# Kernel tuning notes

Measured on AMD Instinct MI355X. Metric: run time of the kernel, lower is better.

The kernel has to match this reference:

```python
import jax, jax.numpy as jnp
import numpy as np

N = 100000   # nodes_num
E = 1600000  # nnz edges (avg degree 16)
F = 256      # input_dim
D = 128      # output_dim
LEAKY_SLOPE = 0.2  # tf.nn.leaky_relu default alpha


def setup_inputs() -> dict:
    key = jax.random.key(0)
    ks = jax.random.split(key, 10)
    x = jax.random.normal(ks[0], (N, F), dtype=jnp.float32)
    adj_vals = jnp.ones((E,), dtype=jnp.float32)
    W_map = jax.random.normal(ks[1], (F, D), dtype=jnp.float32) * 0.05
    w1 = jax.random.normal(ks[2], (D,), dtype=jnp.float32) * 0.05
    b1 = jnp.zeros((1,), dtype=jnp.float32)
    w2 = jax.random.normal(ks[3], (D,), dtype=jnp.float32) * 0.05
    b2 = jnp.zeros((1,), dtype=jnp.float32)
    kernel = jax.random.normal(ks[4], (F, D), dtype=jnp.float32) * 0.05
    bias = jax.random.normal(ks[5], (N, D), dtype=jnp.float32) * 0.05
    edge_row = jnp.sort(jax.random.randint(ks[6], (E,), 0, N, dtype=jnp.int32))
    edge_col = jax.random.randint(ks[7], (E,), 0, N, dtype=jnp.int32)
    return {"x": x, "adj_vals": adj_vals, "W_map": W_map, "w1": w1, "b1": b1,
            "w2": w2, "b2": b2, "kernel": kernel, "bias": bias,
            "edge_row": edge_row, "edge_col": edge_col}


def reference(x, adj_vals, W_map, w1, b1, w2, b2, kernel, bias, edge_row, edge_col):
    # 1x1 Conv1D (no bias) == dense map: [N,F] @ [F,D] -> [N,D]
    mapped = x @ W_map
    # 1x1 Conv1D with bias producing one scalar per node
    sa1 = mapped @ w1 + b1[0]  # [N]
    sa2 = mapped @ w2 + b2[0]  # [N]
    # sparse adj * row-vec + sparse adj * col-vec, then sparse add (same pattern)
    scores = adj_vals * sa1[edge_row] + adj_vals * sa2[edge_col]  # [E]
    scores = jnp.where(scores >= 0, scores, LEAKY_SLOPE * scores)  # leaky_relu
    # sparse row softmax over nonzeros of each row
    row_max = jax.ops.segment_max(scores, edge_row, num_segments=N)  # [N]
    ex = jnp.exp(scores - row_max[edge_row])  # [E]
    denom = jax.ops.segment_sum(ex, edge_row, num_segments=N)  # [N]
    alpha = ex / denom[edge_row]  # [E]
    # value = x @ kernel, then SpMM: out[i] = sum_e alpha_e * value[col_e]
    value = x @ kernel  # [N,D]
    out = jax.ops.segment_sum(alpha[:, None] * value[edge_col], edge_row,
                              num_segments=N)  # [N,D]
    out = out + bias  # use_bias=True
    return out  # activation=None -> linear
```

## Files before the change

kernel.cpp:

```cpp
#include <hip/hip_runtime.h>
#include <math.h>

#define F_DIM 256
#define D_DIM 128
#define LEAKY 0.2f

using bf16x8 = __attribute__((ext_vector_type(8))) short;
using f32x4  = __attribute__((ext_vector_type(4))) float;
using u32x4  = __attribute__((ext_vector_type(4))) unsigned;

__device__ __forceinline__ float wave_sum(float v) {
#pragma unroll
  for (int o = 32; o; o >>= 1) v += __shfl_xor(v, o);
  return v;
}
__device__ __forceinline__ unsigned short f2bf(float f) {
  unsigned u = __float_as_uint(f);
  u += 0x7fffu + ((u >> 16) & 1u);
  return (unsigned short)(u >> 16);
}
__device__ __forceinline__ unsigned cvt2(float lo, float hi) {
  return (unsigned)f2bf(lo) | ((unsigned)f2bf(hi) << 16);
}

__global__ void compute_u_kernel(const float* __restrict__ Wmap,
                                 const float* __restrict__ w1,
                                 const float* __restrict__ w2,
                                 float* __restrict__ u) {
  __shared__ float w1s[D_DIM], w2s[D_DIM];
  int t = threadIdx.x;
  if (t < D_DIM) { w1s[t] = w1[t]; w2s[t] = w2[t]; }
  __syncthreads();
  float a1 = 0.f, a2 = 0.f;
  const float* wp = Wmap + (size_t)t * D_DIM;
#pragma unroll 8
  for (int d = 0; d < D_DIM; ++d) {
    float wv = wp[d];
    a1 += wv * w1s[d];
    a2 += wv * w2s[d];
  }
  u[t] = a1;
  u[F_DIM + t] = a2;
}

__global__ void row_ptr_kernel(const int* __restrict__ edge_row,
                               int* __restrict__ row_ptr, int N, int E) {
  int r = blockIdx.x * blockDim.x + threadIdx.x;
  if (r > N) return;
  int lo = 0, hi = E;
  while (lo < hi) {
    int mid = (lo + hi) >> 1;
    if (edge_row[mid] < r) lo = mid + 1; else hi = mid;
  }
  row_ptr[r] = lo;
}

__global__ void kT_kernel(const float* __restrict__ kern,
                          unsigned short* __restrict__ kTb) {
  int idx = blockIdx.x * blockDim.x + threadIdx.x;
  if (idx >= F_DIM * D_DIM) return;
  int d = idx >> 8;
  int k = idx & 255;
  kTb[d * F_DIM + k] = f2bf(kern[(size_t)k * D_DIM + d]);
}

__global__ __launch_bounds__(256) void value_sa_gemm_kernel(
    const float* __restrict__ x, const unsigned short* __restrict__ kTb,
    const float* __restrict__ u, const float* __restrict__ b1,
    const float* __restrict__ b2, unsigned short* __restrict__ value,
    float* __restrict__ sa1, float* __restrict__ sa2, int N) {
  __shared__ unsigned short ldsb[F_DIM * D_DIM];
  int tid = threadIdx.x;
  int w = tid >> 6, l = tid & 63;
  int rl = l & 15, kg = l >> 4;
  int row = blockIdx.x * 64 + w * 16 + rl;
  bool valid = row < N;
  int rowc = valid ? row : N - 1;

  bf16x8 stg[16];
#pragma unroll
  for (int it = 0; it < 16; ++it)
    stg[it] = *(const bf16x8*)(kTb + (size_t)(tid + it * 256) * 8);

  const float* xp = x + (size_t)rowc * F_DIM + kg * 8;
  float4 fxa[8], fxb[8];
#pragma unroll
  for (int ks = 0; ks < 8; ++ks) {
    fxa[ks] = *(const float4*)(xp + ks * 32);
    fxb[ks] = *(const float4*)(xp + ks * 32 + 4);
  }

#pragma unroll
  for (int it = 0; it < 16; ++it) {
    int c = tid + it * 256;
    int d = c >> 5;
    int sw = d * 512 + (((c & 31) * 16) ^ ((d & 7) << 4));
    *(bf16x8*)((char*)ldsb + sw) = stg[it];
  }

  const float* u1p = u + kg * 8;
  const float* u2p = u + F_DIM + kg * 8;
  float d1 = 0.f, d2 = 0.f;
  bf16x8 af[8];
#pragma unroll
  for (int ks = 0; ks < 8; ++ks) {
    float4 fa = fxa[ks], fb = fxb[ks];
    float4 ua = *(const float4*)(u1p + ks * 32);
    float4 ub = *(const float4*)(u1p + ks * 32 + 4);
    d1 += fa.x * ua.x + fa.y * ua.y + fa.z * ua.z + fa.w * ua.w +
          fb.x * ub.x + fb.y * ub.y + fb.z * ub.z + fb.w * ub.w;
    float4 va = *(const float4*)(u2p + ks * 32);
    float4 vb = *(const float4*)(u2p + ks * 32 + 4);
    d2 += fa.x * va.x + fa.y * va.y + fa.z * va.z + fa.w * va.w +
          fb.x * vb.x + fb.y * vb.y + fb.z * vb.z + fb.w * vb.w;
    u32x4 p;
    p[0] = cvt2(fa.x, fa.y);
    p[1] = cvt2(fa.z, fa.w);
    p[2] = cvt2(fb.x, fb.y);
    p[3] = cvt2(fb.z, fb.w);
    af[ks] = __builtin_bit_cast(bf16x8, p);
  }
  __syncthreads();

  f32x4 acc[8];
#pragma unroll
  for (int n = 0; n < 8; ++n) acc[n] = (f32x4){0.f, 0.f, 0.f, 0.f};
#pragma unroll
  for (int ks = 0; ks < 8; ++ks) {
    int bir = (ks * 64 + kg * 16) ^ ((rl & 7) << 4);
    const char* bp = (const char*)ldsb + rl * 512 + bir;
#pragma unroll
    for (int n = 0; n < 8; ++n) {
      bf16x8 b = *(const bf16x8*)(bp + n * 8192);
      acc[n] = __builtin_amdgcn_mfma_f32_16x16x32_bf16(af[ks], b, acc[n], 0, 0, 0);
    }
  }

  d1 += __shfl_xor(d1, 16); d1 += __shfl_xor(d1, 32);
  d2 += __shfl_xor(d2, 16); d2 += __shfl_xor(d2, 32);
  if (valid && kg == 0) {
    sa1[row] = d1 + b1[0];
    sa2[row] = d2 + b2[0];
  }
  int orow0 = blockIdx.x * 64 + w * 16 + kg * 4;
#pragma unroll
  for (int n = 0; n < 8; ++n) {
#pragma unroll
    for (int i = 0; i < 4; ++i) {
      int gr = orow0 + i;
      if (gr < N) value[(size_t)gr * D_DIM + n * 16 + rl] = f2bf(acc[n][i]);
    }
  }
}

__global__ __launch_bounds__(256) void attn_row_kernel(
    const float* __restrict__ adj, const int* __restrict__ ecol,
    const float* __restrict__ sa1, const float* __restrict__ sa2,
    const int* __restrict__ row_ptr, const unsigned short* __restrict__ value,
    const float* __restrict__ bias, float* __restrict__ out, int N) {
  __shared__ float2 stash[4][64];
  int w = threadIdx.x >> 6;
  int lane = threadIdx.x & 63;
  int r = blockIdx.x * 4 + w;
  if (r >= N) return;
  int s = row_ptr[r], e = row_ptr[r + 1];
  float sa1r = sa1[r];
  int g = lane >> 4;
  int lg = lane & 15;

  float acc0 = 0.f, acc1 = 0.f, acc2 = 0.f, acc3 = 0.f;
  float acc4 = 0.f, acc5 = 0.f, acc6 = 0.f, acc7 = 0.f;
  float l = 0.f;
  const unsigned short* vbase = value + lg * 8;

  for (int base = s; base < e; base += 64) {
    int idx = base + lane;
    float p = 0.f;
    int c = 0;
    if (idx < e) {
      int cc = ecol[idx];
      float a = adj[idx];
      float v = a * sa1r + a * sa2[cc];
      float sc = v >= 0.f ? v : LEAKY * v;
      p = __expf(sc);
      c = cc;
    }
    l += wave_sum(p);
    stash[w][lane] = make_float2(p, __int_as_float(c));
    int cn = e - base;
    if (cn > 64) cn = 64;
    int cn4 = (cn + 3) & ~3;
    for (int j = 0; j < cn4; j += 8) {
      float2 pa = stash[w][j + g];
      bool second = (j + 4 < cn4);
      float2 pb = second ? stash[w][j + 4 + g] : make_float2(0.f, 0.f);
      u32x4 va = *(const u32x4*)(vbase + (size_t)__float_as_int(pa.y) * D_DIM);
      u32x4 vb = *(const u32x4*)(vbase + (size_t)__float_as_int(pb.y) * D_DIM);
      float pja = pa.x, pjb = pb.x;
      acc0 += pja * __uint_as_float(va[0] << 16);
      acc1 += pja * __uint_as_float(va[0] & 0xffff0000u);
      acc2 += pja * __uint_as_float(va[1] << 16);
      acc3 += pja * __uint_as_float(va[1] & 0xffff0000u);
      acc4 += pja * __uint_as_float(va[2] << 16);
      acc5 += pja * __uint_as_float(va[2] & 0xffff0000u);
      acc6 += pja * __uint_as_float(va[3] << 16);
      acc7 += pja * __uint_as_float(va[3] & 0xffff0000u);
      acc0 += pjb * __uint_as_float(vb[0] << 16);
      acc1 += pjb * __uint_as_float(vb[0] & 0xffff0000u);
      acc2 += pjb * __uint_as_float(vb[1] << 16);
      acc3 += pjb * __uint_as_float(vb[1] & 0xffff0000u);
      acc4 += pjb * __uint_as_float(vb[2] << 16);
      acc5 += pjb * __uint_as_float(vb[2] & 0xffff0000u);
      acc6 += pjb * __uint_as_float(vb[3] << 16);
      acc7 += pjb * __uint_as_float(vb[3] & 0xffff0000u);
    }
  }
  acc0 += __shfl_xor(acc0, 16); acc0 += __shfl_xor(acc0, 32);
  acc1 += __shfl_xor(acc1, 16); acc1 += __shfl_xor(acc1, 32);
  acc2 += __shfl_xor(acc2, 16); acc2 += __shfl_xor(acc2, 32);
  acc3 += __shfl_xor(acc3, 16); acc3 += __shfl_xor(acc3, 32);
  acc4 += __shfl_xor(acc4, 16); acc4 += __shfl_xor(acc4, 32);
  acc5 += __shfl_xor(acc5, 16); acc5 += __shfl_xor(acc5, 32);
  acc6 += __shfl_xor(acc6, 16); acc6 += __shfl_xor(acc6, 32);
  acc7 += __shfl_xor(acc7, 16); acc7 += __shfl_xor(acc7, 32);
  float invl = (l > 0.f) ? 1.f / l : 0.f;
  if (g < 2) {
    size_t o = (size_t)r * D_DIM + lg * 8 + g * 4;
    float4 bv = *(const float4*)&bias[o];
    float4 ov;
    ov.x = bv.x + (g == 0 ? acc0 : acc4) * invl;
    ov.y = bv.y + (g == 0 ? acc1 : acc5) * invl;
    ov.z = bv.z + (g == 0 ? acc2 : acc6) * invl;
    ov.w = bv.w + (g == 0 ? acc3 : acc7) * invl;
    *(float4*)&out[o] = ov;
  }
}

extern "C" void kernel_launch(void* const* d_in, const int* in_sizes, int n_in,
                              void* d_out, int out_size, void* d_ws, size_t ws_size,
                              hipStream_t stream) {
  const float* x    = (const float*)d_in[0];
  const float* adj  = (const float*)d_in[1];
  const float* Wmap = (const float*)d_in[2];
  const float* w1   = (const float*)d_in[3];
  const float* b1   = (const float*)d_in[4];
  const float* w2   = (const float*)d_in[5];
  const float* b2   = (const float*)d_in[6];
  const float* kern = (const float*)d_in[7];
  const float* bias = (const float*)d_in[8];
  const int* erow   = (const int*)d_in[9];
  const int* ecol   = (const int*)d_in[10];
  float* out = (float*)d_out;

  int E = in_sizes[1];
  int D = in_sizes[3];
  int F = in_sizes[2] / D;
  int N = in_sizes[0] / F;
  (void)D; (void)ws_size; (void)n_in; (void)out_size;

  char* ws = (char*)d_ws;
  size_t off = 0;
  float* u = (float*)(ws + off);          off += 2 * (size_t)F * sizeof(float);
  float* sa1 = (float*)(ws + off);        off += (size_t)N * sizeof(float);
  float* sa2 = (float*)(ws + off);        off += (size_t)N * sizeof(float);
  int* row_ptr = (int*)(ws + off);        off += (size_t)(N + 1) * sizeof(int);
  off = (off + 255) & ~(size_t)255;
  unsigned short* kTb = (unsigned short*)(ws + off);
  off += (size_t)F_DIM * D_DIM * sizeof(unsigned short);
  off = (off + 255) & ~(size_t)255;
  unsigned short* value = (unsigned short*)(ws + off);
  off += (size_t)N * D_DIM * sizeof(unsigned short);

  compute_u_kernel<<<1, 256, 0, stream>>>(Wmap, w1, w2, u);
  kT_kernel<<<(F_DIM * D_DIM + 255) / 256, 256, 0, stream>>>(kern, kTb);
  row_ptr_kernel<<<(N + 1 + 255) / 256, 256, 0, stream>>>(erow, row_ptr, N, E);
  value_sa_gemm_kernel<<<(N + 63) / 64, 256, 0, stream>>>(x, kTb, u, b1, b2,
                                                          value, sa1, sa2, N);
  attn_row_kernel<<<(N + 3) / 4, 256, 0, stream>>>(adj, ecol, sa1, sa2, row_ptr,
                                                   value, bias, out, N);
}
```

Before: 122.8 us.

## Split attention into alpha packing and column-chunked SpMM kernels

Stores the value matrix in eight 16-column chunk planes instead of row-major order. The fused attention kernel is split in two. One kernel computes the normalized alpha per edge, quantizes it to 15 bits and packs it with the column index into a 32-bit word. A separate SpMM kernel has each block handle one 16-column chunk, so gathers stay within a 3.2MB plane, which is meant to improve cache locality. In exchange it adds a 6.4MB packed-edge round trip and an extra launch. It also loses alpha precision and assumes column indices fit in 17 bits.

```diff
diff --git a/kernel.cpp b/kernel.cpp
--- a/kernel.cpp
+++ b/kernel.cpp
@@ -76,6 +76,7 @@
   int row = blockIdx.x * 64 + w * 16 + rl;
   bool valid = row < N;
   int rowc = valid ? row : N - 1;
+  size_t N16 = (size_t)N * 16;
 
   bf16x8 stg[16];
 #pragma unroll
@@ -148,90 +149,105 @@
 #pragma unroll
     for (int i = 0; i < 4; ++i) {
       int gr = orow0 + i;
-      if (gr < N) value[(size_t)gr * D_DIM + n * 16 + rl] = f2bf(acc[n][i]);
-    }
-  }
-}
-
-__global__ __launch_bounds__(256) void attn_row_kernel(
+      if (gr < N) value[(size_t)n * N16 + (size_t)gr * 16 + rl] = f2bf(acc[n][i]);
+    }
+  }
+}
+
+__global__ __launch_bounds__(256) void alpha_kernel(
     const float* __restrict__ adj, const int* __restrict__ ecol,
     const float* __restrict__ sa1, const float* __restrict__ sa2,
-    const int* __restrict__ row_ptr, const unsigned short* __restrict__ value,
-    const float* __restrict__ bias, float* __restrict__ out, int N) {
-  __shared__ float2 stash[4][64];
+    const int* __restrict__ row_ptr, unsigned* __restrict__ pk, int N) {
   int w = threadIdx.x >> 6;
   int lane = threadIdx.x & 63;
   int r = blockIdx.x * 4 + w;
   if (r >= N) return;
   int s = row_ptr[r], e = row_ptr[r + 1];
+  if (s >= e) return;
   float sa1r = sa1[r];
-  int g = lane >> 4;
-  int lg = lane & 15;
-
-  float acc0 = 0.f, acc1 = 0.f, acc2 = 0.f, acc3 = 0.f;
-  float acc4 = 0.f, acc5 = 0.f, acc6 = 0.f, acc7 = 0.f;
-  float l = 0.f;
-  const unsigned short* vbase = value + lg * 8;
-
-  for (int base = s; base < e; base += 64) {
-    int idx = base + lane;
+  if (e - s <= 64) {
+    int idx = s + lane;
     float p = 0.f;
     int c = 0;
     if (idx < e) {
-      int cc = ecol[idx];
+      c = ecol[idx];
       float a = adj[idx];
-      float v = a * sa1r + a * sa2[cc];
+      float v = a * sa1r + a * sa2[c];
       float sc = v >= 0.f ? v : LEAKY * v;
       p = __expf(sc);
-      c = cc;
-    }
-    l += wave_sum(p);
-    stash[w][lane] = make_float2(p, __int_as_float(c));
-    int cn = e - base;
-    if (cn > 64) cn = 64;
-    int cn4 = (cn + 3) & ~3;
-    for (int j = 0; j < cn4; j += 8) {
-      float2 pa = stash[w][j + g];
-      bool second = (j + 4 < cn4);
-      float2 pb = second ? stash[w][j + 4 + g] : make_float2(0.f, 0.f);
-      u32x4 va = *(const u32x4*)(vbase + (size_t)__float_as_int(pa.y) * D_DIM);
-      u32x4 vb = *(const u32x4*)(vbase + (size_t)__float_as_int(pb.y) * D_DIM);
-      float pja = pa.x, pjb = pb.x;
-      acc0 += pja * __uint_as_float(va[0] << 16);
-      acc1 += pja * __uint_as_float(va[0] & 0xffff0000u);
-      acc2 += pja * __uint_as_float(va[1] << 16);
-      acc3 += pja * __uint_as_float(va[1] & 0xffff0000u);
-      acc4 += pja * __uint_as_float(va[2] << 16);
-      acc5 += pja * __uint_as_float(va[2] & 0xffff0000u);
-      acc6 += pja * __uint_as_float(va[3] << 16);
-      acc7 += pja * __uint_as_float(va[3] & 0xffff0000u);
-      acc0 += pjb * __uint_as_float(vb[0] << 16);
-      acc1 += pjb * __uint_as_float(vb[0] & 0xffff0000u);
-      acc2 += pjb * __uint_as_float(vb[1] << 16);
-      acc3 += pjb * __uint_as_float(vb[1] & 0xffff0000u);
-      acc4 += pjb * __uint_as_float(vb[2] << 16);
-      acc5 += pjb * __uint_as_float(vb[2] & 0xffff0000u);
-      acc6 += pjb * __uint_as_float(vb[3] << 16);
-      acc7 += pjb * __uint_as_float(vb[3] & 0xffff0000u);
-    }
-  }
-  acc0 += __shfl_xor(acc0, 16); acc0 += __shfl_xor(acc0, 32);
-  acc1 += __shfl_xor(acc1, 16); acc1 += __shfl_xor(acc1, 32);
-  acc2 += __shfl_xor(acc2, 16); acc2 += __shfl_xor(acc2, 32);
-  acc3 += __shfl_xor(acc3, 16); acc3 += __shfl_xor(acc3, 32);
-  acc4 += __shfl_xor(acc4, 16); acc4 += __shfl_xor(acc4, 32);
-  acc5 += __shfl_xor(acc5, 16); acc5 += __shfl_xor(acc5, 32);
-  acc6 += __shfl_xor(acc6, 16); acc6 += __shfl_xor(acc6, 32);
-  acc7 += __shfl_xor(acc7, 16); acc7 += __shfl_xor(acc7, 32);
-  float invl = (l > 0.f) ? 1.f / l : 0.f;
-  if (g < 2) {
-    size_t o = (size_t)r * D_DIM + lg * 8 + g * 4;
+    }
+    float l = wave_sum(p);
+    float scale = 32767.f / l;
+    if (idx < e) {
+      unsigned q = (unsigned)fminf(p * scale + 0.5f, 32767.f);
+      pk[idx] = ((unsigned)c << 15) | q;
+    }
+  } else {
+    float l = 0.f;
+    for (int base = s; base < e; base += 64) {
+      int idx = base + lane;
+      float p = 0.f;
+      if (idx < e) {
+        int c = ecol[idx];
+        float a = adj[idx];
+        float v = a * sa1r + a * sa2[c];
+        float sc = v >= 0.f ? v : LEAKY * v;
+        p = __expf(sc);
+      }
+      l += wave_sum(p);
+    }
+    float scale = 32767.f / l;
+    for (int base = s; base < e; base += 64) {
+      int idx = base + lane;
+      if (idx < e) {
+        int c = ecol[idx];
+        float a = adj[idx];
+        float v = a * sa1r + a * sa2[c];
+        float sc = v >= 0.f ? v : LEAKY * v;
+        float p = __expf(sc);
+        unsigned q = (unsigned)fminf(p * scale + 0.5f, 32767.f);
+        pk[idx] = ((unsigned)c << 15) | q;
+      }
+    }
+  }
+}
+
+__global__ __launch_bounds__(256) void spmm_kernel(
+    const unsigned* __restrict__ pk, const int* __restrict__ row_ptr,
+    const unsigned short* __restrict__ value, const float* __restrict__ bias,
+    float* __restrict__ out, int N) {
+  int w = threadIdx.x >> 6;
+  int lane = threadIdx.x & 63;
+  int chunk = blockIdx.x & 7;
+  int r = (blockIdx.x >> 3) * 4 + w;
+  if (r >= N) return;
+  int s = row_ptr[r], e = row_ptr[r + 1];
+  int g = lane >> 2;
+  int q = lane & 3;
+  const unsigned short* vb = value + (size_t)chunk * N * 16 + q * 4;
+  float a0 = 0.f, a1 = 0.f, a2 = 0.f, a3 = 0.f;
+  for (int base = s; base < e; base += 16) {
+    int idx = base + g;
+    unsigned pkv = (idx < e) ? pk[idx] : 0u;
+    float al = (float)(pkv & 32767u) * (1.f / 32767.f);
+    unsigned col = pkv >> 15;
+    uint2 v = *(const uint2*)(vb + (size_t)col * 16);
+    a0 += al * __uint_as_float(v.x << 16);
+    a1 += al * __uint_as_float(v.x & 0xffff0000u);
+    a2 += al * __uint_as_float(v.y << 16);
+    a3 += al * __uint_as_float(v.y & 0xffff0000u);
+  }
+#pragma unroll
+  for (int o = 4; o <= 32; o <<= 1) {
+    a0 += __shfl_xor(a0, o);
+    a1 += __shfl_xor(a1, o);
+    a2 += __shfl_xor(a2, o);
+    a3 += __shfl_xor(a3, o);
+  }
+  if (g == 0) {
+    size_t o = (size_t)r * D_DIM + chunk * 16 + q * 4;
     float4 bv = *(const float4*)&bias[o];
-    float4 ov;
-    ov.x = bv.x + (g == 0 ? acc0 : acc4) * invl;
-    ov.y = bv.y + (g == 0 ? acc1 : acc5) * invl;
-    ov.z = bv.z + (g == 0 ? acc2 : acc6) * invl;
-    ov.w = bv.w + (g == 0 ? acc3 : acc7) * invl;
+    float4 ov = make_float4(bv.x + a0, bv.y + a1, bv.z + a2, bv.w + a3);
     *(float4*)&out[o] = ov;
   }
 }
@@ -268,6 +284,8 @@
   unsigned short* kTb = (unsigned short*)(ws + off);
   off += (size_t)F_DIM * D_DIM * sizeof(unsigned short);
   off = (off + 255) & ~(size_t)255;
+  unsigned* pk = (unsigned*)(ws + off);   off += (size_t)E * sizeof(unsigned);
+  off = (off + 255) & ~(size_t)255;
   unsigned short* value = (unsigned short*)(ws + off);
   off += (size_t)N * D_DIM * sizeof(unsigned short);
 
@@ -276,6 +294,8 @@
   row_ptr_kernel<<<(N + 1 + 255) / 256, 256, 0, stream>>>(erow, row_ptr, N, E);
   value_sa_gemm_kernel<<<(N + 63) / 64, 256, 0, stream>>>(x, kTb, u, b1, b2,
                                                           value, sa1, sa2, N);
-  attn_row_kernel<<<(N + 3) / 4, 256, 0, stream>>>(adj, ecol, sa1, sa2, row_ptr,
-                                                   value, bias, out, N);
-}
+  alpha_kernel<<<(N + 3) / 4, 256, 0, stream>>>(adj, ecol, sa1, sa2, row_ptr,
+                                                pk, N);
+  int rowblks = (N + 3) / 4;
+  spmm_kernel<<<rowblks * 8, 256, 0, stream>>>(pk, row_ptr, value, bias, out, N);
+}
```

New measurement: 301.9 us. 2.46x slower.
